# Performance work log

Hardware: AMD Instinct MI355X
Metric: run time of the kernel (lower is better)

The kernel has to match this reference:

```python
import jax, jax.numpy as jnp
import numpy as np

B, T, D_IDM = 16384, 40, 12
Z_DIM, ACT_DIM, H, ENV = 6, 2, 100, 7
LSTM_IN = H + ACT_DIM + ENV  # 109


def setup_inputs() -> dict:
    key = jax.random.key(0)
    ks = jax.random.split(key, 16)
    s = lambda n: 1.0 / np.sqrt(n)
    return {
        "sampled_z": jax.random.normal(ks[0], (B, Z_DIM), jnp.float32),
        "idm_s": jax.random.uniform(ks[1], (B, T, D_IDM), jnp.float32),
        "sdv_acts": jax.random.normal(ks[2], (B, T, ACT_DIM), jnp.float32),
        "W1": jax.random.normal(ks[3], (Z_DIM, H), jnp.float32) * s(Z_DIM),
        "b1": jnp.zeros((H,), jnp.float32),
        "W2": jax.random.normal(ks[4], (H, H), jnp.float32) * s(H),
        "b2": jnp.zeros((H,), jnp.float32),
        "Wk": jax.random.normal(ks[5], (LSTM_IN, 4 * H), jnp.float32) * s(LSTM_IN),
        "Wr": jax.random.normal(ks[6], (H, 4 * H), jnp.float32) * s(H),
        "bl": jnp.zeros((4 * H,), jnp.float32),
        "Wd": jax.random.normal(ks[7], (H, 1), jnp.float32) * s(H),
        "bd": jnp.zeros((1,), jnp.float32),
        "scaler_mean": jax.random.normal(ks[8], (ENV,), jnp.float32),
        "scaler_var": jax.random.uniform(ks[9], (ENV,), jnp.float32) + 0.5,
    }


def _lstm_cell(x, h, c, Wk, Wr, bl):
    # Keras LSTM gate order: i, f, g(candidate), o
    z = x @ Wk + h @ Wr + bl
    i, f, g, o = jnp.split(z, 4, axis=-1)
    c = jax.nn.sigmoid(f) * c + jax.nn.sigmoid(i) * jnp.tanh(g)
    h = jax.nn.sigmoid(o) * jnp.tanh(c)
    return h, c


def reference(sampled_z, idm_s, sdv_acts, W1, b1, W2, b2, Wk, Wr, bl, Wd, bd, scaler_mean, scaler_var):
    b = sampled_z.shape[0]
    proj = jax.nn.relu(jax.nn.relu(sampled_z @ W1 + b1) @ W2 + b2)  # [B,100]
    inv_std = 1.0 / jnp.sqrt(scaler_var)

    def step(carry, xs):
        h, c, ego_v, ego_x, prev_act = carry
        idm_t, sdv_t, t = xs  # [B,12], [B,2], scalar step index
        is0 = t == 0
        ego_v = jnp.where(is0, idm_t[:, 0:1], ego_v + prev_act * 0.1)
        ego_x = jnp.where(is0, idm_t[:, 3:4], ego_x + ego_v * 0.1 + 0.5 * prev_act * 0.1 ** 2)
        f_veh_v = idm_t[:, 1:2]
        m_veh_v = idm_t[:, 2:3]
        f_glob_x = idm_t[:, 4:5]
        m_glob_x = idm_t[:, 5:6]
        ef_dv_true = idm_t[:, 6:7]
        ef_dx_true = idm_t[:, 7:8]
        em_dv_true = idm_t[:, 8:9]
        em_dx_true = idm_t[:, 9:10]
        f_ex = idm_t[:, -2:-1]
        m_ex = idm_t[:, -1:]
        ef_dx = (f_glob_x - ego_x) * f_ex + (1 - f_ex) * ef_dx_true
        em_dx = (m_glob_x - ego_x) * m_ex + (1 - m_ex) * em_dx_true
        ef_dv = (ego_v - f_veh_v) * f_ex + (1 - f_ex) * ef_dv_true
        em_dv = (ego_v - m_veh_v) * m_ex + (1 - m_ex) * em_dv_true
        env = jnp.concatenate([ego_v, f_veh_v, m_veh_v, ef_dv, ef_dx, em_dv, em_dx], axis=-1)
        env = (env - scaler_mean) * inv_std
        x = jnp.concatenate([proj, sdv_t, env], axis=-1)  # [B,109]
        h, c = _lstm_cell(x, h, c, Wk, Wr, bl)
        act = h @ Wd + bd  # [B,1]
        return (h, c, ego_v, ego_x, act), act

    zeros = jnp.zeros((b, 1), sampled_z.dtype)
    init = (proj, proj, zeros, zeros, zeros)
    xs = (jnp.swapaxes(idm_s, 0, 1), jnp.swapaxes(sdv_acts, 0, 1), jnp.arange(idm_s.shape[1]))
    _, acts = jax.lax.scan(step, init, xs)  # [T,B,1]
    return jnp.swapaxes(acts, 0, 1)  # [B,T,1]
```

## Files before the change

kernel.cpp:

```cpp
#include <hip/hip_runtime.h>

#define TS 40
#define BT 64
#define NT 256
#define NMT 25

typedef short bf16x8 __attribute__((ext_vector_type(8)));
typedef float f32x4 __attribute__((ext_vector_type(4)));
typedef float f32x2 __attribute__((ext_vector_type(2)));

#define W2S_OFF  0
#define H1S_OFF  40000
#define PROJ_OFF 65600
#define SMEM_BYTES 102400

__device__ __forceinline__ unsigned short f2bf(float x) {
    unsigned u = __float_as_uint(x);
    unsigned r = u + 0x7fffu + ((u >> 16) & 1u);
    return (unsigned short)(r >> 16);
}
__device__ __forceinline__ float bf2f(unsigned short s) {
    return __uint_as_float(((unsigned)s) << 16);
}
__device__ __forceinline__ float sigf(float x) {
    return __builtin_amdgcn_rcpf(1.0f + __expf(-x));
}
__device__ __forceinline__ float tanhf_(float x) {
    return 2.0f * __builtin_amdgcn_rcpf(1.0f + __expf(-2.0f * x)) - 1.0f;
}

__global__ void prep_kernel(const float* __restrict__ Wr, const float* __restrict__ Wk,
                            unsigned short* __restrict__ Am, unsigned short* __restrict__ Ah,
                            unsigned short* __restrict__ Al) {
    int gid = blockIdx.x * 256 + threadIdx.x;
    int r = gid >> 7, k = gid & 127;
    int mtr = r >> 4, lgr = (r >> 2) & 3, g = r & 3;
    int col = g * 100 + (4 * mtr + lgr);
    int kc = k >> 5, lgk = (k >> 3) & 3, jj = k & 7;
    float wm = 0.f, wkv = 0.f;
    if (jj <= 6) {
        int mtk = 4 * jj + kc;
        if (mtk <= 24) {
            int su = 4 * mtk + lgk;
            wm  = Wr[su * 400 + col];
            wkv = Wk[su * 400 + col];
        }
    } else {
        int renv = 4 * kc + lgk;
        if (renv <= 8) wm = Wk[(100 + renv) * 400 + col];
    }
    unsigned short hi = f2bf(wkv);
    Am[gid] = f2bf(wm);
    Ah[gid] = hi;
    Al[gid] = f2bf(wkv - bf2f(hi));
}

#define ENV_X9(c0, c1, c2, cs)                                              \
    const float f_veh_v = c0[1], m_veh_v = c0[2];                           \
    const float f_glob_x = c1[0], m_glob_x = c1[1];                         \
    const float ef_dv_t = c1[2], ef_dx_t = c1[3];                           \
    const float em_dv_t = c2[0], em_dx_t = c2[1];                           \
    const float f_ex = c2[2], m_ex = c2[3];                                 \
    const float ef_dx = (f_glob_x - ego_x) * f_ex + (1.f - f_ex) * ef_dx_t; \
    const float em_dx = (m_glob_x - ego_x) * m_ex + (1.f - m_ex) * em_dx_t; \
    const float ef_dv = (ego_v - f_veh_v) * f_ex + (1.f - f_ex) * ef_dv_t;  \
    const float em_dv = (ego_v - m_veh_v) * m_ex + (1.f - m_ex) * em_dv_t;  \
    const float x90 = cs[0], x91 = cs[1];                                   \
    const float x92 = (ego_v   - msr[0]) * isr[0];                          \
    const float x93 = (f_veh_v - msr[1]) * isr[1];                          \
    const float x94 = (m_veh_v - msr[2]) * isr[2];                          \
    const float x95 = (ef_dv   - msr[3]) * isr[3];                          \
    const float x96 = (ef_dx   - msr[4]) * isr[4];                          \
    const float x97 = (em_dv   - msr[5]) * isr[5];                          \
    const float x98 = (em_dx   - msr[6]) * isr[6];

#define PACK_ENV_HI(DH)                                                     \
    {                                                                       \
        const float e0 = (lg==0)?x90:(lg==1)?x91:(lg==2)?x92:x93;           \
        const float e1 = (lg==0)?x94:(lg==1)?x95:(lg==2)?x96:x97;           \
        const float e2 = (lg==0)?x98:0.f;                                   \
        DH[0][7] = (short)f2bf(e0);                                         \
        DH[1][7] = (short)f2bf(e1);                                         \
        DH[2][7] = (short)f2bf(e2);                                         \
        DH[3][7] = 0;                                                       \
    }

__global__ __launch_bounds__(NT, 1)
void fwdsim_kernel(const float* __restrict__ sampled_z,
                   const float* __restrict__ idm_s,
                   const float* __restrict__ sdv_acts,
                   const float* __restrict__ W1, const float* __restrict__ b1,
                   const float* __restrict__ W2, const float* __restrict__ b2,
                   const float* __restrict__ bl, const float* __restrict__ Wd,
                   const float* __restrict__ bd,
                   const float* __restrict__ sc_mean, const float* __restrict__ sc_var,
                   const unsigned short* __restrict__ Am,
                   const unsigned short* __restrict__ Ah,
                   const unsigned short* __restrict__ Al,
                   float* __restrict__ out) {
    __shared__ char sm[SMEM_BYTES];
    float* W2s  = (float*)(sm + W2S_OFF);
    float* h1s  = (float*)(sm + H1S_OFF);
    float* projs= (float*)(sm + PROJ_OFF);

    const int tid = threadIdx.x;
    const int w = tid >> 6, l = tid & 63, lb = l & 15, lg = l >> 4;
    const int blk = blockIdx.x;
    const int bloc = w * 16 + lb;
    const size_t eg = (size_t)(blk * BT + bloc);

    for (int i = tid; i < 2500; i += NT) ((f32x4*)W2s)[i] = ((const f32x4*)W2)[i];
    {
        const int e = tid >> 2, q = tid & 3;
        const int egi = blk * BT + e;
        float zv[6];
        #pragma unroll
        for (int r = 0; r < 6; ++r) zv[r] = sampled_z[egi * 6 + r];
        for (int m = 0; m < 25; ++m) {
            const int c = q * 25 + m;
            float a = b1[c];
            #pragma unroll
            for (int r = 0; r < 6; ++r) a += zv[r] * W1[r * 100 + c];
            h1s[e * 100 + c] = fmaxf(a, 0.f);
        }
    }
    __syncthreads();

    {
        const int e = tid >> 2, q = tid & 3;
        for (int m = 0; m < 25; ++m) {
            const int c = q * 25 + m;
            float a = b2[c];
            for (int k = 0; k < 100; ++k) a += h1s[e * 100 + k] * W2s[k * 100 + c];
            projs[e * 100 + c] = fmaxf(a, 0.f);
        }
    }
    __syncthreads();

    float c_st[NMT], wd_reg[NMT];
    #pragma unroll
    for (int mt = 0; mt < NMT; ++mt) {
        const int u = 4 * mt + lg;
        wd_reg[mt] = Wd[u];
        c_st[mt]   = projs[bloc * 100 + u];
    }

    bf16x8 bh[4], bl_[4];
    #pragma unroll
    for (int kc = 0; kc < 4; ++kc) {
        bh[kc]  = (bf16x8){0,0,0,0,0,0,0,0};
        bl_[kc] = (bf16x8){0,0,0,0,0,0,0,0};
    }
    #pragma unroll
    for (int mt = 0; mt < NMT; ++mt) {
        const int kcq = mt & 3, jjq = mt >> 2;
        const float v = projs[bloc * 100 + 4 * mt + lg];
        const unsigned short hi = f2bf(v);
        bh[kcq][jjq]  = (short)hi;
        bl_[kcq][jjq] = (short)f2bf(v - bf2f(hi));
    }

    float msr[7], isr[7];
    #pragma unroll
    for (int r = 0; r < 7; ++r) { msr[r] = sc_mean[r]; isr[r] = 1.0f / sqrtf(sc_var[r]); }
    const float bd0 = bd[0];

    float gka[NMT * 4];
    #pragma unroll
    for (int mt = 0; mt < NMT; ++mt) {
        f32x4 ac = (f32x4){0.f, 0.f, 0.f, 0.f};
        #pragma unroll
        for (int kc = 0; kc < 4; ++kc) {
            const int row = 16 * mt + lb;
            bf16x8 ah = *(const bf16x8*)(Ah + row * 128 + kc * 32 + lg * 8);
            bf16x8 al = *(const bf16x8*)(Al + row * 128 + kc * 32 + lg * 8);
            ac = __builtin_amdgcn_mfma_f32_16x16x32_bf16(ah, bh[kc],  ac, 0, 0, 0);
            ac = __builtin_amdgcn_mfma_f32_16x16x32_bf16(ah, bl_[kc], ac, 0, 0, 0);
            ac = __builtin_amdgcn_mfma_f32_16x16x32_bf16(al, bh[kc],  ac, 0, 0, 0);
        }
        const int u = 4 * mt + lg;
        const float g0 = ac[0] + bl[u];
        const float g1 = ac[1] + bl[100 + u];
        const float g2 = ac[2] + bl[200 + u];
        const float g3 = ac[3] + bl[300 + u];
        asm volatile("v_accvgpr_write_b32 %0, %1" : "=a"(gka[4 * mt + 0]) : "v"(g0));
        asm volatile("v_accvgpr_write_b32 %0, %1" : "=a"(gka[4 * mt + 1]) : "v"(g1));
        asm volatile("v_accvgpr_write_b32 %0, %1" : "=a"(gka[4 * mt + 2]) : "v"(g2));
        asm volatile("v_accvgpr_write_b32 %0, %1" : "=a"(gka[4 * mt + 3]) : "v"(g3));
    }
    __syncthreads();

    #pragma unroll
    for (int i = 0; i < 25; ++i) {
        const int ch = tid + i * NT;
        const int row = ch >> 4, c16 = ch & 15;
        *(bf16x8*)(sm + row * 256 + ((c16 * 16) ^ ((row & 7) << 4))) =
            *(const bf16x8*)(Am + row * 128 + c16 * 8);
    }
    float ego_v, ego_x;
    f32x4 cur0, cur1, cur2;
    f32x2 curs;
    {
        const float* ip = idm_s + (eg * TS) * 12;
        f32x4 i0 = *(const f32x4*)ip, i1 = *(const f32x4*)(ip + 4), i2 = *(const f32x4*)(ip + 8);
        f32x2 s0 = *(const f32x2*)(sdv_acts + (eg * TS) * 2);
        ego_v = i0[0]; ego_x = i0[3];
        ENV_X9(i0, i1, i2, s0)
        PACK_ENV_HI(bh)
        const float* ip1 = idm_s + (eg * TS + 1) * 12;
        cur0 = *(const f32x4*)ip1; cur1 = *(const f32x4*)(ip1 + 4); cur2 = *(const f32x4*)(ip1 + 8);
        curs = *(const f32x2*)(sdv_acts + (eg * TS + 1) * 2);
    }
    __syncthreads();

    const int sw = (lb & 7) << 4;
    const int k0 = (16 * lg) ^ sw;
    const int k1 = (64 + 16 * lg) ^ sw;
    const int k2 = (128 + 16 * lg) ^ sw;
    const int k3 = (192 + 16 * lg) ^ sw;
    const char* Abase = sm + lb * 256;

    for (int t = 0; t < TS; ++t) {
        bf16x8 nbh[4];
        float pact = 0.f;
        #pragma unroll
        for (int mt = 0; mt < NMT; ++mt) {
            float g0, g1, g2, g3;
            asm("v_accvgpr_read_b32 %0, %1" : "=v"(g0) : "a"(gka[4 * mt + 0]));
            asm("v_accvgpr_read_b32 %0, %1" : "=v"(g1) : "a"(gka[4 * mt + 1]));
            asm("v_accvgpr_read_b32 %0, %1" : "=v"(g2) : "a"(gka[4 * mt + 2]));
            asm("v_accvgpr_read_b32 %0, %1" : "=v"(g3) : "a"(gka[4 * mt + 3]));
            f32x4 ac = (f32x4){g0, g1, g2, g3};
            const char* ap = Abase + mt * 4096;
            bf16x8 a0 = *(const bf16x8*)(ap + k0);
            ac = __builtin_amdgcn_mfma_f32_16x16x32_bf16(a0, bh[0], ac, 0, 0, 0);
            bf16x8 a1 = *(const bf16x8*)(ap + k1);
            ac = __builtin_amdgcn_mfma_f32_16x16x32_bf16(a1, bh[1], ac, 0, 0, 0);
            bf16x8 a2 = *(const bf16x8*)(ap + k2);
            ac = __builtin_amdgcn_mfma_f32_16x16x32_bf16(a2, bh[2], ac, 0, 0, 0);
            bf16x8 a3 = *(const bf16x8*)(ap + k3);
            ac = __builtin_amdgcn_mfma_f32_16x16x32_bf16(a3, bh[3], ac, 0, 0, 0);
            const float cc = sigf(ac[1]) * c_st[mt] + sigf(ac[0]) * tanhf_(ac[2]);
            const float hh = sigf(ac[3]) * tanhf_(cc);
            c_st[mt] = cc;
            pact += hh * wd_reg[mt];
            const int kcq = mt & 3, jjq = mt >> 2;
            nbh[kcq][jjq] = (short)f2bf(hh);
        }
        pact += __shfl_xor(pact, 16);
        pact += __shfl_xor(pact, 32);
        const float act = pact + bd0;
        if (lg == 0) out[eg * TS + t] = act;

        if (t < TS - 1) {
            ego_v += act * 0.1f;
            ego_x += ego_v * 0.1f + 0.005f * act;
            ENV_X9(cur0, cur1, cur2, curs)
            PACK_ENV_HI(nbh)
            nbh[1][6] = 0; nbh[2][6] = 0; nbh[3][6] = 0;
            #pragma unroll
            for (int kc = 0; kc < 4; ++kc) bh[kc] = nbh[kc];
            if (t < TS - 2) {
                const float* ip = idm_s + (eg * TS + t + 2) * 12;
                cur0 = *(const f32x4*)ip; cur1 = *(const f32x4*)(ip + 4); cur2 = *(const f32x4*)(ip + 8);
                curs = *(const f32x2*)(sdv_acts + (eg * TS + t + 2) * 2);
            }
        }
    }
}

extern "C" void kernel_launch(void* const* d_in, const int* in_sizes, int n_in,
                              void* d_out, int out_size, void* d_ws, size_t ws_size,
                              hipStream_t stream) {
    const float* sampled_z = (const float*)d_in[0];
    const float* idm_s     = (const float*)d_in[1];
    const float* sdv_acts  = (const float*)d_in[2];
    const float* W1        = (const float*)d_in[3];
    const float* b1        = (const float*)d_in[4];
    const float* W2        = (const float*)d_in[5];
    const float* b2        = (const float*)d_in[6];
    const float* Wk        = (const float*)d_in[7];
    const float* Wr        = (const float*)d_in[8];
    const float* bl        = (const float*)d_in[9];
    const float* Wd        = (const float*)d_in[10];
    const float* bd        = (const float*)d_in[11];
    const float* sc_mean   = (const float*)d_in[12];
    const float* sc_var    = (const float*)d_in[13];
    float* out = (float*)d_out;

    unsigned short* Am = (unsigned short*)d_ws;
    unsigned short* Ah = Am + 400 * 128;
    unsigned short* Al = Ah + 400 * 128;

    hipLaunchKernelGGL(prep_kernel, dim3(200), dim3(256), 0, stream, Wr, Wk, Am, Ah, Al);
    hipLaunchKernelGGL(fwdsim_kernel, dim3(16384 / BT), dim3(NT), 0, stream,
                       sampled_z, idm_s, sdv_acts, W1, b1, W2, b2, bl, Wd, bd,
                       sc_mean, sc_var, Am, Ah, Al, out);
}
```

Before: 209.5 us.

## Split LSTM gate tiles across two waves per batch tile with LDS h exchange

Doubles the threads per block to 512 and assigns each 16-row batch tile to a pair of waves, each computing about half of the 25 hidden-unit MFMA tiles. Each step, the waves exchange their new bf16 h values and partial output sums through double-buffered LDS and a block-wide barrier. The aim is to shorten the serial per-step chain and raise the number of resident waves (launch bounds now allow 2 blocks per CU). In exchange, every timestep now needs a __syncthreads plus extra LDS traffic, and LDS use per block grows.

```diff
diff --git a/kernel.cpp b/kernel.cpp
--- a/kernel.cpp
+++ b/kernel.cpp
@@ -2,17 +2,19 @@
 
 #define TS 40
 #define BT 64
-#define NT 256
+#define NT 512
 #define NMT 25
 
 typedef short bf16x8 __attribute__((ext_vector_type(8)));
 typedef float f32x4 __attribute__((ext_vector_type(4)));
 typedef float f32x2 __attribute__((ext_vector_type(2)));
 
+#define HX_OFF   102400
+#define PX_OFF   128000
+#define SMEM_BYTES 129024
 #define W2S_OFF  0
 #define H1S_OFF  40000
 #define PROJ_OFF 65600
-#define SMEM_BYTES 102400
 
 __device__ __forceinline__ unsigned short f2bf(float x) {
     unsigned u = __float_as_uint(x);
@@ -85,7 +87,68 @@
         DH[3][7] = 0;                                                       \
     }
 
-__global__ __launch_bounds__(NT, 1)
+#define GK_INIT(MT0, CNT)                                                          \
+    _Pragma("unroll")                                                              \
+    for (int i = 0; i < CNT; ++i) {                                                \
+        const int mt = MT0 + i;                                                    \
+        f32x4 ac = (f32x4){0.f, 0.f, 0.f, 0.f};                                    \
+        _Pragma("unroll")                                                          \
+        for (int kc = 0; kc < 4; ++kc) {                                           \
+            const int row = 16 * mt + lb;                                          \
+            bf16x8 ah = *(const bf16x8*)(Ah + row * 128 + kc * 32 + lg * 8);       \
+            bf16x8 al = *(const bf16x8*)(Al + row * 128 + kc * 32 + lg * 8);       \
+            ac = __builtin_amdgcn_mfma_f32_16x16x32_bf16(ah, bh[kc],  ac, 0,0,0);  \
+            ac = __builtin_amdgcn_mfma_f32_16x16x32_bf16(ah, bl_[kc], ac, 0,0,0);  \
+            ac = __builtin_amdgcn_mfma_f32_16x16x32_bf16(al, bh[kc],  ac, 0,0,0);  \
+        }                                                                          \
+        const int u = 4 * mt + lg;                                                 \
+        const float q0 = ac[0] + bl[u];                                            \
+        const float q1 = ac[1] + bl[100 + u];                                      \
+        const float q2 = ac[2] + bl[200 + u];                                      \
+        const float q3 = ac[3] + bl[300 + u];                                      \
+        asm volatile("v_accvgpr_write_b32 %0, %1" : "=a"(gka[4*i+0]) : "v"(q0));   \
+        asm volatile("v_accvgpr_write_b32 %0, %1" : "=a"(gka[4*i+1]) : "v"(q1));   \
+        asm volatile("v_accvgpr_write_b32 %0, %1" : "=a"(gka[4*i+2]) : "v"(q2));   \
+        asm volatile("v_accvgpr_write_b32 %0, %1" : "=a"(gka[4*i+3]) : "v"(q3));   \
+    }
+
+#define MT_BODY(MT0, CNT)                                                          \
+    _Pragma("unroll")                                                              \
+    for (int i = 0; i < CNT; ++i) {                                                \
+        const int mt = MT0 + i;                                                    \
+        float g0, g1, g2, g3;                                                      \
+        asm("v_accvgpr_read_b32 %0, %1" : "=v"(g0) : "a"(gka[4*i+0]));             \
+        asm("v_accvgpr_read_b32 %0, %1" : "=v"(g1) : "a"(gka[4*i+1]));             \
+        asm("v_accvgpr_read_b32 %0, %1" : "=v"(g2) : "a"(gka[4*i+2]));             \
+        asm("v_accvgpr_read_b32 %0, %1" : "=v"(g3) : "a"(gka[4*i+3]));             \
+        f32x4 ac = (f32x4){g0, g1, g2, g3};                                        \
+        const char* ap = Abase + mt * 4096;                                        \
+        bf16x8 a0 = *(const bf16x8*)(ap + k0);                                     \
+        ac = __builtin_amdgcn_mfma_f32_16x16x32_bf16(a0, bh[0], ac, 0, 0, 0);      \
+        bf16x8 a1 = *(const bf16x8*)(ap + k1);                                     \
+        ac = __builtin_amdgcn_mfma_f32_16x16x32_bf16(a1, bh[1], ac, 0, 0, 0);      \
+        bf16x8 a2 = *(const bf16x8*)(ap + k2);                                     \
+        ac = __builtin_amdgcn_mfma_f32_16x16x32_bf16(a2, bh[2], ac, 0, 0, 0);      \
+        bf16x8 a3 = *(const bf16x8*)(ap + k3);                                     \
+        ac = __builtin_amdgcn_mfma_f32_16x16x32_bf16(a3, bh[3], ac, 0, 0, 0);      \
+        const float cc = sigf(ac[1]) * c_st[i] + sigf(ac[0]) * tanhf_(ac[2]);      \
+        const float hh = sigf(ac[3]) * tanhf_(cc);                                 \
+        c_st[i] = cc;                                                              \
+        pact += hh * wd_reg[i];                                                    \
+        const unsigned short hb = f2bf(hh);                                        \
+        nbh[mt & 3][mt >> 2] = (short)hb;                                          \
+        *(unsigned short*)(sm + HX_OFF + ((((cb*4)+tm)*25 + mt)*64 + lg*16 + lb)*2) = hb; \
+    }
+
+#define OTHER_READ(MT0, CNT)                                                       \
+    _Pragma("unroll")                                                              \
+    for (int i = 0; i < CNT; ++i) {                                                \
+        const int mt = MT0 + i;                                                    \
+        nbh[mt & 3][mt >> 2] = *(const short*)(sm + HX_OFF +                       \
+            ((((cb*4)+tm)*25 + mt)*64 + lg*16 + lb)*2);                            \
+    }
+
+__global__ __launch_bounds__(NT, 2)
 void fwdsim_kernel(const float* __restrict__ sampled_z,
                    const float* __restrict__ idm_s,
                    const float* __restrict__ sdv_acts,
@@ -105,44 +168,57 @@
 
     const int tid = threadIdx.x;
     const int w = tid >> 6, l = tid & 63, lb = l & 15, lg = l >> 4;
+    const int tm = w >> 1, ws = w & 1;
     const int blk = blockIdx.x;
-    const int bloc = w * 16 + lb;
+    const int bloc = tm * 16 + lb;
     const size_t eg = (size_t)(blk * BT + bloc);
 
     for (int i = tid; i < 2500; i += NT) ((f32x4*)W2s)[i] = ((const f32x4*)W2)[i];
     {
-        const int e = tid >> 2, q = tid & 3;
+        const int e = tid >> 3, q = tid & 7;
         const int egi = blk * BT + e;
         float zv[6];
         #pragma unroll
         for (int r = 0; r < 6; ++r) zv[r] = sampled_z[egi * 6 + r];
-        for (int m = 0; m < 25; ++m) {
-            const int c = q * 25 + m;
-            float a = b1[c];
-            #pragma unroll
-            for (int r = 0; r < 6; ++r) a += zv[r] * W1[r * 100 + c];
-            h1s[e * 100 + c] = fmaxf(a, 0.f);
+        #pragma unroll
+        for (int m = 0; m < 13; ++m) {
+            const int c = q * 13 + m;
+            if (c < 100) {
+                float a = b1[c];
+                #pragma unroll
+                for (int r = 0; r < 6; ++r) a += zv[r] * W1[r * 100 + c];
+                h1s[e * 100 + c] = fmaxf(a, 0.f);
+            }
         }
     }
     __syncthreads();
 
     {
-        const int e = tid >> 2, q = tid & 3;
-        for (int m = 0; m < 25; ++m) {
-            const int c = q * 25 + m;
-            float a = b2[c];
-            for (int k = 0; k < 100; ++k) a += h1s[e * 100 + k] * W2s[k * 100 + c];
-            projs[e * 100 + c] = fmaxf(a, 0.f);
+        const int e = tid >> 3, q = tid & 7;
+        for (int m = 0; m < 13; ++m) {
+            const int c = q * 13 + m;
+            if (c < 100) {
+                float a = b2[c];
+                for (int k = 0; k < 100; ++k) a += h1s[e * 100 + k] * W2s[k * 100 + c];
+                projs[e * 100 + c] = fmaxf(a, 0.f);
+            }
         }
     }
     __syncthreads();
 
-    float c_st[NMT], wd_reg[NMT];
-    #pragma unroll
-    for (int mt = 0; mt < NMT; ++mt) {
-        const int u = 4 * mt + lg;
-        wd_reg[mt] = Wd[u];
-        c_st[mt]   = projs[bloc * 100 + u];
+    float c_st[13], wd_reg[13];
+    {
+        const int mt0i = ws * 13, nmw = 13 - ws;
+        #pragma unroll
+        for (int i = 0; i < 13; ++i) { c_st[i] = 0.f; wd_reg[i] = 0.f; }
+        #pragma unroll
+        for (int i = 0; i < 13; ++i) {
+            if (i < nmw) {
+                const int u = 4 * (mt0i + i) + lg;
+                wd_reg[i] = Wd[u];
+                c_st[i]   = projs[bloc * 100 + u];
+            }
+        }
     }
 
     bf16x8 bh[4], bl_[4];
@@ -165,37 +241,18 @@
     for (int r = 0; r < 7; ++r) { msr[r] = sc_mean[r]; isr[r] = 1.0f / sqrtf(sc_var[r]); }
     const float bd0 = bd[0];
 
-    float gka[NMT * 4];
+    float gka[52];
+    if (ws == 0) { GK_INIT(0, 13) } else { GK_INIT(13, 12) }
+    __syncthreads();
+
     #pragma unroll
-    for (int mt = 0; mt < NMT; ++mt) {
-        f32x4 ac = (f32x4){0.f, 0.f, 0.f, 0.f};
-        #pragma unroll
-        for (int kc = 0; kc < 4; ++kc) {
-            const int row = 16 * mt + lb;
-            bf16x8 ah = *(const bf16x8*)(Ah + row * 128 + kc * 32 + lg * 8);
-            bf16x8 al = *(const bf16x8*)(Al + row * 128 + kc * 32 + lg * 8);
-            ac = __builtin_amdgcn_mfma_f32_16x16x32_bf16(ah, bh[kc],  ac, 0, 0, 0);
-            ac = __builtin_amdgcn_mfma_f32_16x16x32_bf16(ah, bl_[kc], ac, 0, 0, 0);
-            ac = __builtin_amdgcn_mfma_f32_16x16x32_bf16(al, bh[kc],  ac, 0, 0, 0);
-        }
-        const int u = 4 * mt + lg;
-        const float g0 = ac[0] + bl[u];
-        const float g1 = ac[1] + bl[100 + u];
-        const float g2 = ac[2] + bl[200 + u];
-        const float g3 = ac[3] + bl[300 + u];
-        asm volatile("v_accvgpr_write_b32 %0, %1" : "=a"(gka[4 * mt + 0]) : "v"(g0));
-        asm volatile("v_accvgpr_write_b32 %0, %1" : "=a"(gka[4 * mt + 1]) : "v"(g1));
-        asm volatile("v_accvgpr_write_b32 %0, %1" : "=a"(gka[4 * mt + 2]) : "v"(g2));
-        asm volatile("v_accvgpr_write_b32 %0, %1" : "=a"(gka[4 * mt + 3]) : "v"(g3));
-    }
-    __syncthreads();
-
-    #pragma unroll
-    for (int i = 0; i < 25; ++i) {
+    for (int i = 0; i < 13; ++i) {
         const int ch = tid + i * NT;
-        const int row = ch >> 4, c16 = ch & 15;
-        *(bf16x8*)(sm + row * 256 + ((c16 * 16) ^ ((row & 7) << 4))) =
-            *(const bf16x8*)(Am + row * 128 + c16 * 8);
+        if (ch < 6400) {
+            const int row = ch >> 4, c16 = ch & 15;
+            *(bf16x8*)(sm + row * 256 + ((c16 * 16) ^ ((row & 7) << 4))) =
+                *(const bf16x8*)(Am + row * 128 + c16 * 8);
+        }
     }
     float ego_v, ego_x;
     f32x4 cur0, cur1, cur2;
@@ -220,42 +277,27 @@
     const int k3 = (192 + 16 * lg) ^ sw;
     const char* Abase = sm + lb * 256;
 
+    int cb = 0;
     for (int t = 0; t < TS; ++t) {
         bf16x8 nbh[4];
         float pact = 0.f;
-        #pragma unroll
-        for (int mt = 0; mt < NMT; ++mt) {
-            float g0, g1, g2, g3;
-            asm("v_accvgpr_read_b32 %0, %1" : "=v"(g0) : "a"(gka[4 * mt + 0]));
-            asm("v_accvgpr_read_b32 %0, %1" : "=v"(g1) : "a"(gka[4 * mt + 1]));
-            asm("v_accvgpr_read_b32 %0, %1" : "=v"(g2) : "a"(gka[4 * mt + 2]));
-            asm("v_accvgpr_read_b32 %0, %1" : "=v"(g3) : "a"(gka[4 * mt + 3]));
-            f32x4 ac = (f32x4){g0, g1, g2, g3};
-            const char* ap = Abase + mt * 4096;
-            bf16x8 a0 = *(const bf16x8*)(ap + k0);
-            ac = __builtin_amdgcn_mfma_f32_16x16x32_bf16(a0, bh[0], ac, 0, 0, 0);
-            bf16x8 a1 = *(const bf16x8*)(ap + k1);
-            ac = __builtin_amdgcn_mfma_f32_16x16x32_bf16(a1, bh[1], ac, 0, 0, 0);
-            bf16x8 a2 = *(const bf16x8*)(ap + k2);
-            ac = __builtin_amdgcn_mfma_f32_16x16x32_bf16(a2, bh[2], ac, 0, 0, 0);
-            bf16x8 a3 = *(const bf16x8*)(ap + k3);
-            ac = __builtin_amdgcn_mfma_f32_16x16x32_bf16(a3, bh[3], ac, 0, 0, 0);
-            const float cc = sigf(ac[1]) * c_st[mt] + sigf(ac[0]) * tanhf_(ac[2]);
-            const float hh = sigf(ac[3]) * tanhf_(cc);
-            c_st[mt] = cc;
-            pact += hh * wd_reg[mt];
-            const int kcq = mt & 3, jjq = mt >> 2;
-            nbh[kcq][jjq] = (short)f2bf(hh);
-        }
+        if (ws == 0) { MT_BODY(0, 13) } else { MT_BODY(13, 12) }
         pact += __shfl_xor(pact, 16);
         pact += __shfl_xor(pact, 32);
-        const float act = pact + bd0;
-        if (lg == 0) out[eg * TS + t] = act;
+        if (l < 16)
+            *(float*)(sm + PX_OFF + ((((cb*4)+tm)*2 + ws)*16 + l) * 4) = pact;
+        __syncthreads();
+
+        const float p0 = *(const float*)(sm + PX_OFF + ((((cb*4)+tm)*2 + 0)*16 + lb) * 4);
+        const float p1 = *(const float*)(sm + PX_OFF + ((((cb*4)+tm)*2 + 1)*16 + lb) * 4);
+        const float act = p0 + p1 + bd0;
+        if (ws == 0 && lg == 0) out[eg * TS + t] = act;
 
         if (t < TS - 1) {
             ego_v += act * 0.1f;
             ego_x += ego_v * 0.1f + 0.005f * act;
             ENV_X9(cur0, cur1, cur2, curs)
+            if (ws == 0) { OTHER_READ(13, 12) } else { OTHER_READ(0, 13) }
             PACK_ENV_HI(nbh)
             nbh[1][6] = 0; nbh[2][6] = 0; nbh[3][6] = 0;
             #pragma unroll
@@ -266,6 +308,7 @@
                 curs = *(const f32x2*)(sdv_acts + (eg * TS + t + 2) * 2);
             }
         }
+        cb ^= 1;
     }
 }
 
```

Measured after the change: 222.0 us. +6.0%, slower.
